# Performance work log

Measured on AMD Instinct MI355X. Metric: run time of the kernel, lower is better.

The kernel has to match this reference:

```python
import jax, jax.numpy as jnp
import numpy as np

D_MODEL, D_STATE, D_CONV, EXPAND, MLP_EXPAND = 1024, 16, 4, 2, 2
D_INNER = EXPAND * D_MODEL          # 2048
DT_RANK = D_MODEL // 16             # 64
B, L = 2, 1024


def setup_inputs() -> dict:
    key = jax.random.key(0)
    ks = jax.random.split(key, 16)
    s = 0.02
    inp = {
        "x": jax.random.normal(ks[0], (B, L, D_MODEL), jnp.float32),
        "ln1_w": jnp.ones((D_MODEL,), jnp.float32),
        "ln1_b": jnp.zeros((D_MODEL,), jnp.float32),
        "in_proj_w": jax.random.normal(ks[1], (2 * D_INNER, D_MODEL), jnp.float32) * s,
        "conv_w": jax.random.normal(ks[2], (D_INNER, 1, D_CONV), jnp.float32) * s,
        "conv_b": jnp.zeros((D_INNER,), jnp.float32),
        "x_proj_w": jax.random.normal(ks[3], (DT_RANK + 2 * D_STATE, D_INNER), jnp.float32) * s,
        "dt_proj_w": jax.random.normal(ks[4], (D_INNER, DT_RANK), jnp.float32) * s,
        "dt_proj_b": jax.random.uniform(ks[5], (D_INNER,), jnp.float32, -4.0, -2.0),
        "A_log": jnp.tile(jnp.log(jnp.arange(1, D_STATE + 1, dtype=jnp.float32))[None, :], (D_INNER, 1)),
        "D": jnp.ones((D_INNER,), jnp.float32),
        "out_proj_w": jax.random.normal(ks[6], (D_MODEL, D_INNER), jnp.float32) * s,
        "ln2_w": jnp.ones((D_MODEL,), jnp.float32),
        "ln2_b": jnp.zeros((D_MODEL,), jnp.float32),
        "mlp_w1": jax.random.normal(ks[7], (MLP_EXPAND * D_MODEL, D_MODEL), jnp.float32) * s,
        "mlp_b1": jnp.zeros((MLP_EXPAND * D_MODEL,), jnp.float32),
        "mlp_w2": jax.random.normal(ks[8], (D_MODEL, MLP_EXPAND * D_MODEL), jnp.float32) * s,
        "mlp_b2": jnp.zeros((D_MODEL,), jnp.float32),
    }
    return inp


def _layernorm(x, w, b, eps=1e-5):
    mu = jnp.mean(x, -1, keepdims=True)
    var = jnp.var(x, -1, keepdims=True)
    return (x - mu) * jax.lax.rsqrt(var + eps) * w + b


def _mamba(x, in_proj_w, conv_w, conv_b, x_proj_w, dt_proj_w, dt_proj_b, A_log, D, out_proj_w):
    # x: (B, L, d_model)
    xz = jnp.einsum('bld,ed->ble', x, in_proj_w)          # (B, L, 2*d_inner)
    u, z = jnp.split(xz, 2, axis=-1)                      # each (B, L, d_inner)
    # depthwise causal conv over time
    u_c = jnp.transpose(u, (0, 2, 1))                     # (B, d_inner, L)
    u_c = jax.lax.conv_general_dilated(
        u_c, conv_w, window_strides=(1,), padding=[(D_CONV - 1, 0)],
        dimension_numbers=('NCH', 'OIH', 'NCH'), feature_group_count=D_INNER)
    u = jax.nn.silu(jnp.transpose(u_c, (0, 2, 1)) + conv_b)  # (B, L, d_inner)

    dbc = jnp.einsum('bld,ed->ble', u, x_proj_w)          # (B, L, dt_rank+2*d_state)
    dt, Bm, Cm = jnp.split(dbc, [DT_RANK, DT_RANK + D_STATE], axis=-1)
    delta = jax.nn.softplus(jnp.einsum('blr,dr->bld', dt, dt_proj_w) + dt_proj_b)  # (B, L, d_inner)

    A = -jnp.exp(A_log)                                   # (d_inner, d_state)
    deltaA = jnp.exp(delta[..., None] * A)                # (B, L, d_inner, d_state)
    deltaBu = delta[..., None] * Bm[:, :, None, :] * u[..., None]

    def step(h, inp):
        dA, dBu, Ct = inp
        h = dA * h + dBu                                  # (B, d_inner, d_state)
        y = jnp.einsum('bdn,bn->bd', h, Ct)
        return h, y

    h0 = jnp.zeros((x.shape[0], D_INNER, D_STATE), x.dtype)
    xs = (jnp.moveaxis(deltaA, 1, 0), jnp.moveaxis(deltaBu, 1, 0), jnp.moveaxis(Cm, 1, 0))
    _, ys = jax.lax.scan(step, h0, xs)                    # (L, B, d_inner)
    y = jnp.moveaxis(ys, 0, 1) + u * D                    # (B, L, d_inner)
    y = y * jax.nn.silu(z)
    return jnp.einsum('ble,de->bld', y, out_proj_w)


def reference(x, ln1_w, ln1_b, in_proj_w, conv_w, conv_b, x_proj_w, dt_proj_w, dt_proj_b,
              A_log, D, out_proj_w, ln2_w, ln2_b, mlp_w1, mlp_b1, mlp_w2, mlp_b2):
    h = x + _mamba(_layernorm(x, ln1_w, ln1_b), in_proj_w, conv_w, conv_b,
                   x_proj_w, dt_proj_w, dt_proj_b, A_log, D, out_proj_w)
    y = _layernorm(h, ln2_w, ln2_b)
    y = jax.nn.gelu(jnp.einsum('bld,ed->ble', y, mlp_w1) + mlp_b1, approximate=False)
    y = jnp.einsum('ble,de->bld', y, mlp_w2) + mlp_b2
    return h + y
```

## Files before the change

kernel.cpp:

```cpp
#include <hip/hip_runtime.h>
#include <hip/hip_bf16.h>
#include <math.h>

typedef __hip_bfloat16 bf16;
typedef __attribute__((ext_vector_type(8))) short bf16x8;
typedef __attribute__((ext_vector_type(4))) float f32x4;

__device__ __forceinline__ float b2f(bf16 x) { return __bfloat162float(x); }
__device__ __forceinline__ float us2f(unsigned short u) {
    return __uint_as_float(((unsigned int)u) << 16);
}
__device__ __forceinline__ unsigned short f2us(float f) {
    bf16 t = __float2bfloat16(f);
    return *reinterpret_cast<unsigned short*>(&t);
}
__device__ __forceinline__ float scrub(float v) {
    return (v == v && fabsf(v) < 3.0e38f) ? v : 0.f;
}
__device__ __forceinline__ float to_float(float x) { return x; }
__device__ __forceinline__ float to_float(bf16 x) { return __bfloat162float(x); }
__device__ __forceinline__ void store_out(float* p, float v) { *p = v; }
__device__ __forceinline__ void store_out(bf16* p, float v) { *p = __float2bfloat16(v); }

__device__ __forceinline__ void cp16(const void* g, void* l) {
    __builtin_amdgcn_global_load_lds(
        (const __attribute__((address_space(1))) unsigned int*)g,
        (__attribute__((address_space(3))) unsigned int*)l, 16, 0, 0);
}

struct Ptrs { const void* p[18]; };

__constant__ __device__ const long TOFF[19] = {
    0,         2097152,  2098176,  2099200,  6293504,  6301696,  6303744,
    6500352,   6631424,  6633472,  6666240,  6668288,  8765440,  8766464,
    8767488,   10864640, 10866688, 12963840, 12964864};

__global__ __launch_bounds__(256) void convert_kernel(
    Ptrs ptrs, unsigned short* __restrict__ dst)
{
    const long g = (long)blockIdx.x * 256 + threadIdx.x;
    if (g >= 1620608) return;
    const long e0 = g * 8;
    int t = 0;
    #pragma unroll
    for (int i = 1; i < 18; ++i) t += (e0 >= TOFF[i]) ? 1 : 0;
    const long local = e0 - TOFF[t];
    const float4* ps = (const float4*)((const float*)ptrs.p[t] + local);
    const float4 a = ps[0], b = ps[1];
    ushort4 o0, o1;
    o0.x = f2us(a.x); o0.y = f2us(a.y); o0.z = f2us(a.z); o0.w = f2us(a.w);
    o1.x = f2us(b.x); o1.y = f2us(b.y); o1.z = f2us(b.z); o1.w = f2us(b.w);
    *(ushort4*)(dst + e0)     = o0;
    *(ushort4*)(dst + e0 + 4) = o1;
}

template <typename TIN>
__global__ __launch_bounds__(256) void ln_kernel(
    const TIN* __restrict__ in, const bf16* __restrict__ gw,
    const bf16* __restrict__ gb, bf16* __restrict__ out)
{
    const int row = blockIdx.x;
    const int tid = threadIdx.x;
    float v[4];
    if constexpr (sizeof(TIN) == 2) {
        ushort4 raw = ((const ushort4*)((const unsigned short*)in + (long)row * 1024))[tid];
        v[0] = us2f(raw.x); v[1] = us2f(raw.y); v[2] = us2f(raw.z); v[3] = us2f(raw.w);
    } else {
        float4 raw = ((const float4*)((const float*)in + (long)row * 1024))[tid];
        v[0] = raw.x; v[1] = raw.y; v[2] = raw.z; v[3] = raw.w;
    }
    float s  = v[0] + v[1] + v[2] + v[3];
    float s2 = v[0]*v[0] + v[1]*v[1] + v[2]*v[2] + v[3]*v[3];
    #pragma unroll
    for (int o = 32; o > 0; o >>= 1) {
        s  += __shfl_xor(s, o);
        s2 += __shfl_xor(s2, o);
    }
    __shared__ float red[8];
    if ((tid & 63) == 0) { red[tid >> 6] = s; red[4 + (tid >> 6)] = s2; }
    __syncthreads();
    s  = red[0] + red[1] + red[2] + red[3];
    s2 = red[4] + red[5] + red[6] + red[7];
    const float mu  = s * (1.f / 1024.f);
    const float var = fmaxf(s2 * (1.f / 1024.f) - mu * mu, 0.f);
    const float rs  = rsqrtf(var + 1e-5f);
    const int c0 = tid * 4;
    ushort4 o;
    o.x = f2us((v[0] - mu) * rs * b2f(gw[c0 + 0]) + b2f(gb[c0 + 0]));
    o.y = f2us((v[1] - mu) * rs * b2f(gw[c0 + 1]) + b2f(gb[c0 + 1]));
    o.z = f2us((v[2] - mu) * rs * b2f(gw[c0 + 2]) + b2f(gb[c0 + 2]));
    o.w = f2us((v[3] - mu) * rs * b2f(gw[c0 + 3]) + b2f(gb[c0 + 3]));
    ((ushort4*)((unsigned short*)out + (long)row * 1024))[tid] = o;
}

template <int BM, int BN, int ACT, bool NG, int SK, typename TOUT, typename TRES>
__global__ __launch_bounds__(256) void gemm_as(
    const bf16* __restrict__ A, int lda,
    const bf16* __restrict__ Bw, int ldb,
    TOUT* __restrict__ C, int ldc,
    const bf16* __restrict__ bias,
    const TRES* __restrict__ res,
    int M, int N, int K)
{
    constexpr int AI = BM / 32;
    constexpr int BJ = BN / 32;
    __shared__ __align__(16) short As[BM * 64];
    __shared__ __align__(16) short Bs[BN * 64];
    const int tid  = threadIdx.x;
    const int lane = tid & 63;
    const int wv   = tid >> 6;
    const int m0 = blockIdx.y * BM;
    const int n0 = blockIdx.x * BN;
    if (SK > 1) {
        const int bz = blockIdx.z;
        A  += (long)bz * K;
        Bw += (long)bz * K;
        C  += (long)bz * M * (long)ldc;
    }
    const int wm = (wv >> 1) * (BM / 2);
    const int wn = (wv & 1) * (BN / 2);
    const int lr = lane & 15;
    const int lq = lane >> 4;
    const int grow = lane >> 3;
    const int gcol = (lane & 7) * 8;

    if (NG) {
        const int z0 = (N - n0) * 64;
        uint4 z; z.x = z.y = z.z = z.w = 0;
        for (int s = z0 + tid * 8; s < BN * 64; s += 2048)
            *(uint4*)&Bs[s] = z;
    }

    f32x4 acc[AI][BJ] = {};

    for (int k0 = 0; k0 < K; k0 += 64) {
        #pragma unroll
        for (int g = 0; g < BM / 32; ++g) {
            const int gg = g * 4 + wv;
            cp16(A + (long)(m0 + gg * 8 + grow) * lda + k0 + gcol, &As[gg * 512]);
        }
        #pragma unroll
        for (int g = 0; g < BN / 32; ++g) {
            const int gg = g * 4 + wv;
            if (!NG || n0 + gg * 8 < N)
                cp16(Bw + (long)(n0 + gg * 8 + grow) * ldb + k0 + gcol, &Bs[gg * 512]);
        }
        __syncthreads();

        #pragma unroll
        for (int kk = 0; kk < 2; ++kk) {
            bf16x8 af[AI], bfr[BJ];
            #pragma unroll
            for (int i = 0; i < AI; ++i)
                af[i] = *(const bf16x8*)&As[(wm + i * 16 + lr) * 64 + kk * 32 + lq * 8];
            #pragma unroll
            for (int j = 0; j < BJ; ++j)
                bfr[j] = *(const bf16x8*)&Bs[(wn + j * 16 + lr) * 64 + kk * 32 + lq * 8];
            #pragma unroll
            for (int i = 0; i < AI; ++i)
                #pragma unroll
                for (int j = 0; j < BJ; ++j)
                    acc[i][j] = __builtin_amdgcn_mfma_f32_16x16x32_bf16(
                        af[i], bfr[j], acc[i][j], 0, 0, 0);
        }
        __syncthreads();
    }

    #pragma unroll
    for (int j = 0; j < BJ; ++j) {
        const int col = n0 + wn + j * 16 + lr;
        if (col >= N) continue;
        const float bv = bias ? b2f(bias[col]) : 0.f;
        #pragma unroll
        for (int i = 0; i < AI; ++i) {
            const int r0 = m0 + wm + i * 16 + lq * 4;
            #pragma unroll
            for (int r = 0; r < 4; ++r) {
                const long row = r0 + r;
                float v = acc[i][j][r] + bv;
                if (ACT == 1) v = 0.5f * v * (1.f + erff(v * 0.70710678118f));
                if (ACT == 2) v = (v > 20.f) ? v : log1pf(__expf(v));
                if (res) v += to_float(res[row * (long)ldc + col]);
                store_out(&C[row * (long)ldc + col], scrub(v));
            }
        }
    }
}

__global__ __launch_bounds__(256) void splitk_reduce_kernel(
    const float* __restrict__ part, bf16* __restrict__ out)
{
    const int i = blockIdx.x * 256 + threadIdx.x;
    if (i >= 196608) return;
    float s = 0.f;
    #pragma unroll
    for (int z = 0; z < 8; ++z) s += part[(long)z * 196608 + i];
    out[i] = __float2bfloat16(s);
}

__global__ __launch_bounds__(256) void conv_silu_kernel(
    const bf16* __restrict__ xz, const bf16* __restrict__ cw,
    const bf16* __restrict__ cb, bf16* __restrict__ ucz)
{
    const int gid = blockIdx.x * 256 + threadIdx.x;
    const int d   = gid & 2047;
    const int row = gid >> 11;
    const int t   = row & 1023;
    float acc = b2f(cb[d]);
    #pragma unroll
    for (int j = 0; j < 4; ++j) {
        const int tt = t - 3 + j;
        if (tt >= 0)
            acc += b2f(cw[d * 4 + j]) * b2f(xz[(long)(row - 3 + j) * 4096 + d]);
    }
    ucz[(long)row * 4096 + d] = __float2bfloat16(acc / (1.f + __expf(-acc)));
    const float zz = b2f(xz[(long)row * 4096 + 2048 + d]);
    ucz[(long)row * 4096 + 2048 + d] = __float2bfloat16(zz / (1.f + __expf(-zz)));
}

__device__ __forceinline__ int swizzle_d0(int bx) {
    return ((bx & 7) << 8) | ((bx >> 3) << 4);
}

__global__ __launch_bounds__(256) void scan_local_kernel(
    const bf16* __restrict__ delta,
    const bf16* __restrict__ ucz,
    const bf16* __restrict__ dbc,
    const float* __restrict__ A_log,
    const float* __restrict__ Dp,
    bf16* __restrict__ y_local,
    bf16* __restrict__ Pbuf,
    float* __restrict__ h_out)
{
    const int d0  = swizzle_d0(blockIdx.x);
    const int b   = blockIdx.y;
    const int sg  = blockIdx.z;
    const int tid = threadIdx.x;
    const int n   = tid & 15;
    const int dl  = tid >> 4;
    const int d   = d0 + dl;

    __shared__ float2         sDU[32][16];
    __shared__ float2         sBC[32][16];
    __shared__ float          sZ [32][16];
    __shared__ unsigned short sPc[32][16];
    __shared__ unsigned short sY [32][16];
    __shared__ float          sP [16 * 648];

    const float An = -expf(A_log[d * 16 + n]);
    const float Dd = Dp[d];
    float h = 0.f, Pc = 0.f;
    const long rowbase = (long)b * 1024 + sg * 128;

    const int wv  = tid >> 6;
    const int pdl = 4 * wv + ((tid & 63) >> 4);
    const int ptq = tid & 15;

    float rDT[2], rUV[2], rZ[2], rBC[4];
    auto load_chunk = [&](int t0c) {
        #pragma unroll
        for (int k = 0; k < 2; ++k) {
            const int i  = k * 256 + tid;
            const int tt = i >> 4, dd = i & 15;
            const long r = rowbase + t0c + tt;
            rDT[k] = b2f(delta[r * 2048 + d0 + dd]);
            rUV[k] = b2f(ucz  [r * 4096 + d0 + dd]);
            rZ[k]  = b2f(ucz  [r * 4096 + 2048 + d0 + dd]);
        }
        #pragma unroll
        for (int k = 0; k < 4; ++k) {
            const int i  = k * 256 + tid;
            const int tt = i >> 5, c = i & 31;
            rBC[k] = b2f(dbc[(rowbase + t0c + tt) * 96 + 64 + c]);
        }
    };
    auto store_chunk = [&]() {
        #pragma unroll
        for (int k = 0; k < 2; ++k) {
            const int i  = k * 256 + tid;
            const int tt = i >> 4, dd = i & 15;
            sDU[tt][dd] = float2{rDT[k], rUV[k]};
            sZ[tt][dd]  = rZ[k];
        }
        #pragma unroll
        for (int k = 0; k < 4; ++k) {
            const int i  = k * 256 + tid;
            const int tt = i >> 5, c = i & 31;
            ((float*)&sBC[tt][0])[(c & 15) * 2 + (c >> 4)] = rBC[k];
        }
    };

    load_chunk(0);
    for (int t0 = 0; t0 < 128; t0 += 32) {
        store_chunk();
        __syncthreads();
        if (t0 + 32 < 128) load_chunk(t0 + 32);

        #pragma unroll 4
        for (int t = 0; t < 32; ++t) {
            const float2 du = sDU[t][dl];
            const float2 bc = sBC[t][n];
            Pc += du.x;
            const float a = __expf(du.x * An);
            h = a * h + (du.x * du.y) * bc.x;
            float p = h * bc.y;
            if (n == 0) { p += du.y * Dd; sPc[t][dl] = f2us(Pc); }
            sP[dl * 648 + t * 20 + n] = p;
        }

        #pragma unroll
        for (int k = 0; k < 2; ++k) {
            const int t = ptq + k * 16;
            const float4* pp = (const float4*)&sP[pdl * 648 + t * 20];
            const float4 p0 = pp[0], p1 = pp[1], p2 = pp[2], p3 = pp[3];
            const float s = ((p0.x + p0.y) + (p0.z + p0.w))
                          + ((p1.x + p1.y) + (p1.z + p1.w))
                          + ((p2.x + p2.y) + (p2.z + p2.w))
                          + ((p3.x + p3.y) + (p3.z + p3.w));
            sY[t][pdl] = f2us(s * sZ[t][pdl]);
        }
        __syncthreads();

        #pragma unroll
        for (int k = 0; k < 2; ++k) {
            const int i  = k * 256 + tid;
            const int tt = i >> 4, dd = i & 15;
            const long r = rowbase + t0 + tt;
            ((unsigned short*)y_local)[r * 2048 + d0 + dd] = sY[tt][dd];
            ((unsigned short*)Pbuf)  [r * 2048 + d0 + dd] = sPc[tt][dd];
        }
        __syncthreads();
    }

    h_out[((long)(b * 8 + sg) * 2048 + d) * 16 + n] = h;
}

__global__ __launch_bounds__(256) void scan_combine_kernel(
    const bf16*  __restrict__ Pbuf,
    const float* __restrict__ A_log,
    const float* __restrict__ h_out,
    float* __restrict__ h_in)
{
    const int gid = blockIdx.x * 256 + threadIdx.x;
    const int b  = gid >> 15;
    const int dn = gid & 32767;
    const int d  = dn >> 4;
    const float An = -expf(A_log[dn]);
    float hin = 0.f;
    h_in[(long)(b * 8) * 32768 + dn] = 0.f;
    for (int s = 0; s < 7; ++s) {
        const float Pend = us2f(((const unsigned short*)Pbuf)
                                [((long)b * 1024 + s * 128 + 127) * 2048 + d]);
        const float hout = h_out[(long)(b * 8 + s) * 32768 + dn];
        hin = hout + __expf(An * Pend) * hin;
        h_in[(long)(b * 8 + s + 1) * 32768 + dn] = hin;
    }
}

__global__ __launch_bounds__(256) void scan_fix_kernel(
    bf16* __restrict__ y,
    const bf16* __restrict__ Pbuf,
    const bf16* __restrict__ dbc,
    const bf16* __restrict__ ucz,
    const float* __restrict__ A_log,
    const float* __restrict__ h_in)
{
    const int d0  = swizzle_d0(blockIdx.x);
    const int b   = blockIdx.y;
    const int sg  = blockIdx.z;
    const int tid = threadIdx.x;
    const long rowb = (long)b * 1024 + sg * 128;

    __shared__ float sH [16][16];
    __shared__ float sAn[16][16];
    __shared__ float sCc[128][16];

    sH [tid >> 4][tid & 15] = h_in[(long)(b * 8 + sg) * 32768 + d0 * 16 + tid];
    sAn[tid >> 4][tid & 15] = -expf(A_log[d0 * 16 + tid]);
    for (int i = tid; i < 2048; i += 256)
        sCc[i >> 4][i & 15] = b2f(dbc[(rowb + (i >> 4)) * 96 + 80 + (i & 15)]);
    __syncthreads();

    const int dd = tid & 15;
    float4 An4[4], H4[4];
    #pragma unroll
    for (int j = 0; j < 4; ++j) {
        An4[j] = *(const float4*)&sAn[dd][j * 4];
        H4[j]  = *(const float4*)&sH [dd][j * 4];
    }

    #pragma unroll
    for (int k = 0; k < 8; ++k) {
        const int t = k * 16 + (tid >> 4);
        const long row = rowb + t;
        const float P = us2f(((const unsigned short*)Pbuf)[row * 2048 + d0 + dd]);
        float corr = 0.f;
        #pragma unroll
        for (int j = 0; j < 4; ++j) {
            const float4 C4 = *(const float4*)&sCc[t][j * 4];
            corr += C4.x * __expf(An4[j].x * P) * H4[j].x;
            corr += C4.y * __expf(An4[j].y * P) * H4[j].y;
            corr += C4.z * __expf(An4[j].z * P) * H4[j].z;
            corr += C4.w * __expf(An4[j].w * P) * H4[j].w;
        }
        const float slz = b2f(ucz[row * 4096 + 2048 + d0 + dd]);
        const float yl  = b2f(y[row * 2048 + d0 + dd]);
        y[row * 2048 + d0 + dd] = __float2bfloat16(yl + slz * corr);
    }
}

extern "C" void kernel_launch(void* const* d_in, const int* in_sizes, int n_in,
                              void* d_out, int out_size, void* d_ws, size_t ws_size,
                              hipStream_t stream)
{
    char* ws = (char*)d_ws;
    const size_t MiB = 1048576;
    const size_t HMiB = 524288;

    bf16*  ucz  = (bf16*)(ws);
    bf16*  dbc  = (bf16*)(ws + 16 * MiB);
    bf16*  xn   = (bf16*)(ws + 16 * MiB + HMiB);
    bf16*  dlb  = (bf16*)(ws + 16 * MiB + HMiB);
    bf16*  xz   = (bf16*)(ws + 20 * MiB + HMiB);
    float* xpart= (float*)(ws + 20 * MiB + HMiB);
    bf16*  Pbuf = (bf16*)(ws + 24 * MiB + HMiB);
    float* hout = (float*)(ws + 32 * MiB + HMiB);
    float* hin  = (float*)(ws + 34 * MiB + HMiB);
    float* hb   = (float*)(ws);
    bf16*  hn   = (bf16*)(ws +  8 * MiB);
    bf16*  gb   = (bf16*)(ws + 24 * MiB + HMiB);
    unsigned short* cvt = (unsigned short*)(ws + 37 * MiB);

    const float* xf     = (const float*)d_in[0];
    const float* A_logf = (const float*)d_in[9];
    const float* Dpf    = (const float*)d_in[10];

    const bf16* ln1_w      = (const bf16*)(cvt + 2097152);
    const bf16* ln1_b      = (const bf16*)(cvt + 2098176);
    const bf16* in_proj_w  = (const bf16*)(cvt + 2099200);
    const bf16* conv_w     = (const bf16*)(cvt + 6293504);
    const bf16* conv_b     = (const bf16*)(cvt + 6301696);
    const bf16* x_proj_w   = (const bf16*)(cvt + 6303744);
    const bf16* dt_proj_w  = (const bf16*)(cvt + 6500352);
    const bf16* dt_proj_b  = (const bf16*)(cvt + 6631424);
    const bf16* out_proj_w = (const bf16*)(cvt + 6668288);
    const bf16* ln2_w      = (const bf16*)(cvt + 8765440);
    const bf16* ln2_b      = (const bf16*)(cvt + 8766464);
    const bf16* mlp_w1     = (const bf16*)(cvt + 8767488);
    const bf16* mlp_b1     = (const bf16*)(cvt + 10864640);
    const bf16* mlp_w2     = (const bf16*)(cvt + 10866688);
    const bf16* mlp_b2     = (const bf16*)(cvt + 12963840);

    Ptrs ptrs;
    for (int i = 0; i < 18; ++i) ptrs.p[i] = d_in[i];
    convert_kernel<<<6332, 256, 0, stream>>>(ptrs, cvt);

    ln_kernel<float><<<2048, 256, 0, stream>>>(xf, ln1_w, ln1_b, xn);
    gemm_as<128, 128, 0, false, 1, bf16, bf16><<<dim3(32, 16), 256, 0, stream>>>(
        xn, 1024, in_proj_w, 1024, xz, 4096, nullptr, (const bf16*)nullptr, 2048, 4096, 1024);
    conv_silu_kernel<<<16384, 256, 0, stream>>>(xz, conv_w, conv_b, ucz);
    gemm_as<64, 64, 0, true, 8, float, bf16><<<dim3(2, 32, 8), 256, 0, stream>>>(
        ucz, 4096, x_proj_w, 2048, xpart, 96, nullptr, (const bf16*)nullptr, 2048, 96, 256);
    splitk_reduce_kernel<<<768, 256, 0, stream>>>(xpart, dbc);
    gemm_as<128, 64, 2, false, 1, bf16, bf16><<<dim3(32, 16), 256, 0, stream>>>(
        dbc, 96, dt_proj_w, 64, dlb, 2048, dt_proj_b, (const bf16*)nullptr, 2048, 2048, 64);
    scan_local_kernel<<<dim3(128, 2, 8), 256, 0, stream>>>(
        dlb, ucz, dbc, A_logf, Dpf, dlb, Pbuf, hout);
    scan_combine_kernel<<<256, 256, 0, stream>>>(Pbuf, A_logf, hout, hin);
    scan_fix_kernel<<<dim3(128, 2, 8), 256, 0, stream>>>(
        dlb, Pbuf, dbc, ucz, A_logf, hin);
    gemm_as<64, 64, 0, false, 1, float, float><<<dim3(16, 32), 256, 0, stream>>>(
        dlb, 2048, out_proj_w, 2048, hb, 1024, nullptr, xf, 2048, 1024, 2048);
    ln_kernel<float><<<2048, 256, 0, stream>>>(hb, ln2_w, ln2_b, hn);
    gemm_as<128, 64, 1, false, 1, bf16, bf16><<<dim3(32, 16), 256, 0, stream>>>(
        hn, 1024, mlp_w1, 1024, gb, 2048, mlp_b1, (const bf16*)nullptr, 2048, 2048, 1024);
    gemm_as<64, 64, 0, false, 1, float, float><<<dim3(16, 32), 256, 0, stream>>>(
        gb, 2048, mlp_w2, 2048, (float*)d_out, 1024, mlp_b2, hb, 2048, 1024, 2048);
}
```

Baseline: 370.5 us.

## Split scan into 32 shorter segments and vectorize conv-silu kernel

The chunked selective scan now uses 32 segments of 32 timesteps instead of 8 of 128. This gives four times as many blocks for the local and fix passes and shortens each serial dependency chain. The chunk-boundary states go into one bf16 buffer that the combine kernel updates in place, though the combine kernel now walks 32 segments serially. The conv+SiLU kernel is also rewritten so each thread handles 8 channels with vector loads and stores. The risks are that boundary states are held in bf16, which costs precision, and that the combine chain is longer.

Result: no change. 364.1 us (-1.7%).

```diff
diff --git a/kernel.cpp b/kernel.cpp
--- a/kernel.cpp
+++ b/kernel.cpp
@@ -21,6 +21,13 @@
 __device__ __forceinline__ float to_float(bf16 x) { return __bfloat162float(x); }
 __device__ __forceinline__ void store_out(float* p, float v) { *p = v; }
 __device__ __forceinline__ void store_out(bf16* p, float v) { *p = __float2bfloat16(v); }
+
+__device__ __forceinline__ void ld8(const bf16* p, float* f) {
+    const ushort4 a = ((const ushort4*)p)[0];
+    const ushort4 b = ((const ushort4*)p)[1];
+    f[0]=us2f(a.x); f[1]=us2f(a.y); f[2]=us2f(a.z); f[3]=us2f(a.w);
+    f[4]=us2f(b.x); f[5]=us2f(b.y); f[6]=us2f(b.z); f[7]=us2f(b.w);
+}
 
 __device__ __forceinline__ void cp16(const void* g, void* l) {
     __builtin_amdgcn_global_load_lds(
@@ -203,19 +210,51 @@
     const bf16* __restrict__ cb, bf16* __restrict__ ucz)
 {
     const int gid = blockIdx.x * 256 + threadIdx.x;
-    const int d   = gid & 2047;
-    const int row = gid >> 11;
+    const int row = gid >> 8;
     const int t   = row & 1023;
-    float acc = b2f(cb[d]);
+    const int d   = (gid & 255) * 8;
+
+    float w[32];
+    ld8(cw + d * 4,      w);
+    ld8(cw + d * 4 + 8,  w + 8);
+    ld8(cw + d * 4 + 16, w + 16);
+    ld8(cw + d * 4 + 24, w + 24);
+
+    float acc[8];
+    ld8(cb + d, acc);
     #pragma unroll
     for (int j = 0; j < 4; ++j) {
         const int tt = t - 3 + j;
-        if (tt >= 0)
-            acc += b2f(cw[d * 4 + j]) * b2f(xz[(long)(row - 3 + j) * 4096 + d]);
-    }
-    ucz[(long)row * 4096 + d] = __float2bfloat16(acc / (1.f + __expf(-acc)));
-    const float zz = b2f(xz[(long)row * 4096 + 2048 + d]);
-    ucz[(long)row * 4096 + 2048 + d] = __float2bfloat16(zz / (1.f + __expf(-zz)));
+        if (tt >= 0) {
+            float u[8];
+            ld8(xz + (long)(row - 3 + j) * 4096 + d, u);
+            #pragma unroll
+            for (int k = 0; k < 8; ++k) acc[k] += w[k * 4 + j] * u[k];
+        }
+    }
+    ushort4 o0, o1;
+    unsigned short* po = (unsigned short*)&o0;
+    #pragma unroll
+    for (int k = 0; k < 8; ++k) {
+        const float v = acc[k] / (1.f + __expf(-acc[k]));
+        ((unsigned short*)&o0)[k & 3 | ((k >> 2) << 31)] = 0;
+        if (k < 4) ((unsigned short*)&o0)[k] = f2us(v);
+        else       ((unsigned short*)&o1)[k - 4] = f2us(v);
+    }
+    (void)po;
+    ((ushort4*)(ucz + (long)row * 4096 + d))[0] = o0;
+    ((ushort4*)(ucz + (long)row * 4096 + d))[1] = o1;
+
+    float z8[8];
+    ld8(xz + (long)row * 4096 + 2048 + d, z8);
+    #pragma unroll
+    for (int k = 0; k < 8; ++k) {
+        const float v = z8[k] / (1.f + __expf(-z8[k]));
+        if (k < 4) ((unsigned short*)&o0)[k] = f2us(v);
+        else       ((unsigned short*)&o1)[k - 4] = f2us(v);
+    }
+    ((ushort4*)(ucz + (long)row * 4096 + 2048 + d))[0] = o0;
+    ((ushort4*)(ucz + (long)row * 4096 + 2048 + d))[1] = o1;
 }
 
 __device__ __forceinline__ int swizzle_d0(int bx) {
@@ -230,7 +269,7 @@
     const float* __restrict__ Dp,
     bf16* __restrict__ y_local,
     bf16* __restrict__ Pbuf,
-    float* __restrict__ h_out)
+    bf16* __restrict__ H)
 {
     const int d0  = swizzle_d0(blockIdx.x);
     const int b   = blockIdx.y;
@@ -245,59 +284,40 @@
     __shared__ float          sZ [32][16];
     __shared__ unsigned short sPc[32][16];
     __shared__ unsigned short sY [32][16];
-    __shared__ float          sP [16 * 648];
+    __shared__ float          sP [16 * 336];
 
     const float An = -expf(A_log[d * 16 + n]);
     const float Dd = Dp[d];
-    float h = 0.f, Pc = 0.f;
-    const long rowbase = (long)b * 1024 + sg * 128;
+    const long rowbase = (long)b * 1024 + sg * 32;
 
     const int wv  = tid >> 6;
     const int pdl = 4 * wv + ((tid & 63) >> 4);
     const int ptq = tid & 15;
 
-    float rDT[2], rUV[2], rZ[2], rBC[4];
-    auto load_chunk = [&](int t0c) {
-        #pragma unroll
-        for (int k = 0; k < 2; ++k) {
-            const int i  = k * 256 + tid;
-            const int tt = i >> 4, dd = i & 15;
-            const long r = rowbase + t0c + tt;
-            rDT[k] = b2f(delta[r * 2048 + d0 + dd]);
-            rUV[k] = b2f(ucz  [r * 4096 + d0 + dd]);
-            rZ[k]  = b2f(ucz  [r * 4096 + 2048 + d0 + dd]);
-        }
-        #pragma unroll
-        for (int k = 0; k < 4; ++k) {
-            const int i  = k * 256 + tid;
-            const int tt = i >> 5, c = i & 31;
-            rBC[k] = b2f(dbc[(rowbase + t0c + tt) * 96 + 64 + c]);
-        }
-    };
-    auto store_chunk = [&]() {
-        #pragma unroll
-        for (int k = 0; k < 2; ++k) {
-            const int i  = k * 256 + tid;
-            const int tt = i >> 4, dd = i & 15;
-            sDU[tt][dd] = float2{rDT[k], rUV[k]};
-            sZ[tt][dd]  = rZ[k];
-        }
-        #pragma unroll
-        for (int k = 0; k < 4; ++k) {
-            const int i  = k * 256 + tid;
-            const int tt = i >> 5, c = i & 31;
-            ((float*)&sBC[tt][0])[(c & 15) * 2 + (c >> 4)] = rBC[k];
-        }
-    };
-
-    load_chunk(0);
-    for (int t0 = 0; t0 < 128; t0 += 32) {
-        store_chunk();
-        __syncthreads();
-        if (t0 + 32 < 128) load_chunk(t0 + 32);
-
+    #pragma unroll
+    for (int k = 0; k < 2; ++k) {
+        const int i  = k * 256 + tid;
+        const int tt = i >> 4, dd = i & 15;
+        const long r = rowbase + tt;
+        sDU[tt][dd] = float2{b2f(delta[r * 2048 + d0 + dd]),
+                             b2f(ucz  [r * 4096 + d0 + dd])};
+        sZ[tt][dd]  = b2f(ucz[r * 4096 + 2048 + d0 + dd]);
+    }
+    #pragma unroll
+    for (int k = 0; k < 4; ++k) {
+        const int i  = k * 256 + tid;
+        const int tt = i >> 5, c = i & 31;
+        ((float*)&sBC[tt][0])[(c & 15) * 2 + (c >> 4)] =
+            b2f(dbc[(rowbase + tt) * 96 + 64 + c]);
+    }
+    __syncthreads();
+
+    float h = 0.f, Pc = 0.f;
+    #pragma unroll
+    for (int half = 0; half < 2; ++half) {
         #pragma unroll 4
-        for (int t = 0; t < 32; ++t) {
+        for (int tl = 0; tl < 16; ++tl) {
+            const int t = half * 16 + tl;
             const float2 du = sDU[t][dl];
             const float2 bc = sBC[t][n];
             Pc += du.x;
@@ -305,13 +325,11 @@
             h = a * h + (du.x * du.y) * bc.x;
             float p = h * bc.y;
             if (n == 0) { p += du.y * Dd; sPc[t][dl] = f2us(Pc); }
-            sP[dl * 648 + t * 20 + n] = p;
-        }
-
-        #pragma unroll
-        for (int k = 0; k < 2; ++k) {
-            const int t = ptq + k * 16;
-            const float4* pp = (const float4*)&sP[pdl * 648 + t * 20];
+            sP[dl * 336 + tl * 20 + n] = p;
+        }
+        {
+            const int t = half * 16 + ptq;
+            const float4* pp = (const float4*)&sP[pdl * 336 + ptq * 20];
             const float4 p0 = pp[0], p1 = pp[1], p2 = pp[2], p3 = pp[3];
             const float s = ((p0.x + p0.y) + (p0.z + p0.w))
                           + ((p1.x + p1.y) + (p1.z + p1.w))
@@ -319,27 +337,25 @@
                           + ((p3.x + p3.y) + (p3.z + p3.w));
             sY[t][pdl] = f2us(s * sZ[t][pdl]);
         }
-        __syncthreads();
-
-        #pragma unroll
-        for (int k = 0; k < 2; ++k) {
-            const int i  = k * 256 + tid;
-            const int tt = i >> 4, dd = i & 15;
-            const long r = rowbase + t0 + tt;
-            ((unsigned short*)y_local)[r * 2048 + d0 + dd] = sY[tt][dd];
-            ((unsigned short*)Pbuf)  [r * 2048 + d0 + dd] = sPc[tt][dd];
-        }
-        __syncthreads();
-    }
-
-    h_out[((long)(b * 8 + sg) * 2048 + d) * 16 + n] = h;
+    }
+    __syncthreads();
+
+    #pragma unroll
+    for (int k = 0; k < 2; ++k) {
+        const int i  = k * 256 + tid;
+        const int tt = i >> 4, dd = i & 15;
+        const long r = rowbase + tt;
+        ((unsigned short*)y_local)[r * 2048 + d0 + dd] = sY[tt][dd];
+        ((unsigned short*)Pbuf)  [r * 2048 + d0 + dd] = sPc[tt][dd];
+    }
+
+    H[((long)(b * 32 + sg) * 2048 + d) * 16 + n] = __float2bfloat16(h);
 }
 
 __global__ __launch_bounds__(256) void scan_combine_kernel(
     const bf16*  __restrict__ Pbuf,
     const float* __restrict__ A_log,
-    const float* __restrict__ h_out,
-    float* __restrict__ h_in)
+    bf16* __restrict__ H)
 {
     const int gid = blockIdx.x * 256 + threadIdx.x;
     const int b  = gid >> 15;
@@ -347,13 +363,12 @@
     const int d  = dn >> 4;
     const float An = -expf(A_log[dn]);
     float hin = 0.f;
-    h_in[(long)(b * 8) * 32768 + dn] = 0.f;
-    for (int s = 0; s < 7; ++s) {
-        const float Pend = us2f(((const unsigned short*)Pbuf)
-                                [((long)b * 1024 + s * 128 + 127) * 2048 + d]);
-        const float hout = h_out[(long)(b * 8 + s) * 32768 + dn];
+    for (int s = 0; s < 32; ++s) {
+        const long idx = (long)(b * 32 + s) * 32768 + dn;
+        const float hout = b2f(H[idx]);
+        H[idx] = __float2bfloat16(hin);
+        const float Pend = b2f(Pbuf[((long)b * 1024 + s * 32 + 31) * 2048 + d]);
         hin = hout + __expf(An * Pend) * hin;
-        h_in[(long)(b * 8 + s + 1) * 32768 + dn] = hin;
     }
 }
 
@@ -363,21 +378,21 @@
     const bf16* __restrict__ dbc,
     const bf16* __restrict__ ucz,
     const float* __restrict__ A_log,
-    const float* __restrict__ h_in)
+    const bf16* __restrict__ H)
 {
     const int d0  = swizzle_d0(blockIdx.x);
     const int b   = blockIdx.y;
     const int sg  = blockIdx.z;
     const int tid = threadIdx.x;
-    const long rowb = (long)b * 1024 + sg * 128;
+    const long rowb = (long)b * 1024 + sg * 32;
 
     __shared__ float sH [16][16];
     __shared__ float sAn[16][16];
-    __shared__ float sCc[128][16];
-
-    sH [tid >> 4][tid & 15] = h_in[(long)(b * 8 + sg) * 32768 + d0 * 16 + tid];
+    __shared__ float sCc[32][16];
+
+    sH [tid >> 4][tid & 15] = b2f(H[(long)(b * 32 + sg) * 32768 + d0 * 16 + tid]);
     sAn[tid >> 4][tid & 15] = -expf(A_log[d0 * 16 + tid]);
-    for (int i = tid; i < 2048; i += 256)
+    for (int i = tid; i < 512; i += 256)
         sCc[i >> 4][i & 15] = b2f(dbc[(rowb + (i >> 4)) * 96 + 80 + (i & 15)]);
     __syncthreads();
 
@@ -390,7 +405,7 @@
     }
 
     #pragma unroll
-    for (int k = 0; k < 8; ++k) {
+    for (int k = 0; k < 2; ++k) {
         const int t = k * 16 + (tid >> 4);
         const long row = rowb + t;
         const float P = us2f(((const unsigned short*)Pbuf)[row * 2048 + d0 + dd]);
@@ -424,8 +439,7 @@
     bf16*  xz   = (bf16*)(ws + 20 * MiB + HMiB);
     float* xpart= (float*)(ws + 20 * MiB + HMiB);
     bf16*  Pbuf = (bf16*)(ws + 24 * MiB + HMiB);
-    float* hout = (float*)(ws + 32 * MiB + HMiB);
-    float* hin  = (float*)(ws + 34 * MiB + HMiB);
+    bf16*  Hbuf = (bf16*)(ws + 32 * MiB + HMiB);
     float* hb   = (float*)(ws);
     bf16*  hn   = (bf16*)(ws +  8 * MiB);
     bf16*  gb   = (bf16*)(ws + 24 * MiB + HMiB);
@@ -458,17 +472,17 @@
     ln_kernel<float><<<2048, 256, 0, stream>>>(xf, ln1_w, ln1_b, xn);
     gemm_as<128, 128, 0, false, 1, bf16, bf16><<<dim3(32, 16), 256, 0, stream>>>(
         xn, 1024, in_proj_w, 1024, xz, 4096, nullptr, (const bf16*)nullptr, 2048, 4096, 1024);
-    conv_silu_kernel<<<16384, 256, 0, stream>>>(xz, conv_w, conv_b, ucz);
+    conv_silu_kernel<<<2048, 256, 0, stream>>>(xz, conv_w, conv_b, ucz);
     gemm_as<64, 64, 0, true, 8, float, bf16><<<dim3(2, 32, 8), 256, 0, stream>>>(
         ucz, 4096, x_proj_w, 2048, xpart, 96, nullptr, (const bf16*)nullptr, 2048, 96, 256);
     splitk_reduce_kernel<<<768, 256, 0, stream>>>(xpart, dbc);
     gemm_as<128, 64, 2, false, 1, bf16, bf16><<<dim3(32, 16), 256, 0, stream>>>(
         dbc, 96, dt_proj_w, 64, dlb, 2048, dt_proj_b, (const bf16*)nullptr, 2048, 2048, 64);
-    scan_local_kernel<<<dim3(128, 2, 8), 256, 0, stream>>>(
-        dlb, ucz, dbc, A_logf, Dpf, dlb, Pbuf, hout);
-    scan_combine_kernel<<<256, 256, 0, stream>>>(Pbuf, A_logf, hout, hin);
-    scan_fix_kernel<<<dim3(128, 2, 8), 256, 0, stream>>>(
-        dlb, Pbuf, dbc, ucz, A_logf, hin);
+    scan_local_kernel<<<dim3(128, 2, 32), 256, 0, stream>>>(
+        dlb, ucz, dbc, A_logf, Dpf, dlb, Pbuf, Hbuf);
+    scan_combine_kernel<<<256, 256, 0, stream>>>(Pbuf, A_logf, Hbuf);
+    scan_fix_kernel<<<dim3(128, 2, 32), 256, 0, stream>>>(
+        dlb, Pbuf, dbc, ucz, A_logf, Hbuf);
     gemm_as<64, 64, 0, false, 1, float, float><<<dim3(16, 32), 256, 0, stream>>>(
         dlb, 2048, out_proj_w, 2048, hb, 1024, nullptr, xf, 2048, 1024, 2048);
     ln_kernel<float><<<2048, 256, 0, stream>>>(hb, ln2_w, ln2_b, hn);
```
